# Optimization experiments

Measured on AMD Instinct MI355X. Metric: run time of the kernel, lower is better.

The kernel has to match this reference:

```python
import jax, jax.numpy as jnp
import numpy as np

B = 262144   # batch of candidate user-item pairs
D = 256      # concat embedding dim (embedding_dim*8)
H = 128      # hypernet hidden
HD = 32      # expert hidden dim
E = 4        # num experts


def setup_inputs() -> dict:
    key = jax.random.key(0)
    ks = jax.random.split(key, 16)
    def w(k, shape, fan_in):
        return jax.random.normal(k, shape, jnp.float32) * (1.0 / np.sqrt(fan_in))
    return {
        "x": jax.random.normal(ks[0], (B, D), jnp.float32),
        "context_embed": jax.random.normal(ks[1], (D,), jnp.float32),
        # hypernet (soft_module_route)
        "W1": w(ks[2], (D, H), D),   "b1": jnp.zeros((H,), jnp.float32),
        "W2": w(ks[3], (H, H), H),   "b2": jnp.zeros((H,), jnp.float32),
        "W12": w(ks[4], (H, E * E), H), "b12": jnp.zeros((E * E,), jnp.float32),
        "W22": w(ks[5], (H, E), H),     "b22": jnp.zeros((E,), jnp.float32),
        # soft_module experts: stacked per-expert Linear weights
        "Wf1": w(ks[6], (E, D, HD), D), "bf1": jnp.zeros((E, HD), jnp.float32),
        "Wf2": w(ks[7], (E, HD, HD), HD), "bf2": jnp.zeros((E, HD), jnp.float32),
        "Wfin": w(ks[8], (HD, 1), HD),  "bfin": jnp.zeros((1,), jnp.float32),
    }


def reference(x, context_embed, W1, b1, W2, b2, W12, b12, W22, b22,
              Wf1, bf1, Wf2, bf2, Wfin, bfin):
    # hypernet: routing weights from x * context
    embeds = x * context_embed[None, :]                       # [B,D]
    h = jax.nn.relu(embeds @ W1 + b1)                         # [B,H]
    c1 = jax.nn.softmax((h @ W12 + b12).reshape(-1, E, E), axis=1)   # [B,4,4]
    h2 = jax.nn.relu(h @ W2 + b2)                             # [B,H]
    c2 = jax.nn.softmax((h2 @ W22 + b22).reshape(-1, E, 1), axis=1)  # [B,4,1]
    # soft_module: 4 experts per layer, soft combined via c1/c2
    o1 = jax.nn.relu(jnp.einsum('bd,edh->bhe', x, Wf1) + bf1.T)      # [B,HD,E]
    in2 = jnp.einsum('bhe,bef->bhf', o1, c1)                         # [B,HD,E]
    o2 = jax.nn.relu(jnp.einsum('bhe,ehk->bke', in2, Wf2) + bf2.T)   # [B,HD,E]
    in3 = jnp.einsum('bke,bef->bkf', o2, c2)[..., 0]                 # [B,HD]
    return in3 @ Wfin + bfin                                         # [B,1]
```

## Files before the change

kernel.cpp:

```cpp
#include <hip/hip_runtime.h>
#include <hip/hip_bf16.h>

typedef _Float16 f16;
typedef _Float16 half8 __attribute__((ext_vector_type(8)));
typedef _Float16 half4 __attribute__((ext_vector_type(4)));
typedef float floatx4 __attribute__((ext_vector_type(4)));

#define BM 64

#define WA_OFF 0
#define WB_OFF 65536
#define WC_OFF 83968
#define WF2_OFF 86016
#define WSF_BYTE_OFF 180224
#define BA_OFF 0
#define BB_OFF 256
#define BCC_OFF 400
#define BF2_OFF 404
#define WFIN_OFF 532
#define BFIN_OFF 564

__global__ __launch_bounds__(256) void prep_kernel(
    const float* __restrict__ ctx, const float* __restrict__ W1,
    const float* __restrict__ b1, const float* __restrict__ W2,
    const float* __restrict__ b2, const float* __restrict__ W12,
    const float* __restrict__ b12, const float* __restrict__ W22,
    const float* __restrict__ b22, const float* __restrict__ Wf1,
    const float* __restrict__ bf1, const float* __restrict__ Wf2,
    const float* __restrict__ bf2, const float* __restrict__ Wfin,
    const float* __restrict__ bfin, f16* __restrict__ wsh,
    float* __restrict__ wsf)
{
  int tid = blockIdx.x * 256 + threadIdx.x;
  if (tid < 65536) {
    int j = tid & 7, l = (tid >> 3) & 63, kt = (tid >> 9) & 7, nt = tid >> 12;
    int k = kt * 32 + ((l >> 4) << 3) + j, n = nt * 16 + (l & 15);
    float v;
    if (n < 128) v = ctx[k] * W1[k * 128 + n];
    else { int c = n - 128; v = Wf1[((c >> 5) * 256 + k) * 32 + (c & 31)]; }
    wsh[tid] = (f16)v;
  } else if (tid < WB_OFF + 18432) {
    int o = tid - WB_OFF;
    int j = o & 7, l = (o >> 3) & 63, kt = (o >> 9) & 3, nt = o >> 11;
    int k = kt * 32 + ((l >> 4) << 3) + j, n = nt * 16 + (l & 15);
    float v = (n < 128) ? W2[k * 128 + n] : W12[k * 16 + (n - 128)];
    wsh[tid] = (f16)v;
  } else if (tid < WC_OFF + 2048) {
    int o = tid - WC_OFF;
    int j = o & 7, l = (o >> 3) & 63, kt = (o >> 9) & 3;
    int k = kt * 32 + ((l >> 4) << 3) + j, n = l & 15;
    float v = (n < 4) ? W22[k * 4 + n] : 0.f;
    wsh[tid] = (f16)v;
  } else if (tid < WF2_OFF + 4096) {
    int o = tid - WF2_OFF;
    int j = o & 7, l = (o >> 3) & 63, ent = o >> 9;
    int e = ent >> 1, nt = ent & 1;
    int k = ((l >> 4) << 3) + j, n = nt * 16 + (l & 15);
    wsh[tid] = (f16)Wf2[(e * 32 + k) * 32 + n];
  } else if (tid < 90112 + 565) {
    int o = tid - 90112;
    float v;
    if (o < 128) v = b1[o];
    else if (o < 256) v = bf1[o - 128];
    else if (o < 384) v = b2[o - 256];
    else if (o < 400) v = b12[o - 384];
    else if (o < 404) v = b22[o - 400];
    else if (o < 532) v = bf2[o - 404];
    else if (o < 564) v = Wfin[o - 532];
    else v = bfin[0];
    wsf[o] = v;
  }
}

#define MFMA16(A, Bv, C) __builtin_amdgcn_mfma_f32_16x16x32_f16(A, Bv, C, 0, 0, 0)

#define L1_OFF 32768
#define PART_OFF 32768
#define C2_OFF 34816

__global__ __launch_bounds__(256, 3) void fused_kernel(
    const float* __restrict__ x, const f16* __restrict__ wsh,
    const float* __restrict__ wsf, float* __restrict__ out)
{
  __shared__ __attribute__((aligned(16))) char lds[35840];
  const int t = threadIdx.x;
  const int lane = t & 63;
  const int w = t >> 6;
  const int l15 = lane & 15;
  const int l4 = lane >> 4;
  const size_t base = (size_t)blockIdx.x * BM;

#pragma unroll
  for (int it = 0; it < 8; ++it) {
    int c = it * 256 + t;
    int r = c >> 5;
    int k0 = (c & 31) << 3;
    const float4* xv = (const float4*)(x + (base + (size_t)r) * 256 + k0);
    float4 a = xv[0], b = xv[1];
    half8 hv;
    hv[0] = (f16)a.x; hv[1] = (f16)a.y; hv[2] = (f16)a.z; hv[3] = (f16)a.w;
    hv[4] = (f16)b.x; hv[5] = (f16)b.y; hv[6] = (f16)b.z; hv[7] = (f16)b.w;
    int addr = (r * 512 + k0 * 2) ^ ((r & 7) << 4);
    *(half8*)(lds + addr) = hv;
  }
  __syncthreads();

  {
    floatx4 acc[4][4];
#pragma unroll
    for (int q = 0; q < 4; ++q)
#pragma unroll
      for (int mt = 0; mt < 4; ++mt) acc[q][mt] = (floatx4){0.f, 0.f, 0.f, 0.f};
    for (int kt = 0; kt < 8; ++kt) {
      half8 Bx[4];
#pragma unroll
      for (int mt = 0; mt < 4; ++mt) {
        int r = mt * 16 + l15;
        int addr = (r * 512 + kt * 64 + (l4 << 4)) ^ ((r & 7) << 4);
        Bx[mt] = *(const half8*)(lds + addr);
      }
#pragma unroll
      for (int q = 0; q < 4; ++q) {
        half8 Wf = *(const half8*)(wsh + WA_OFF + (size_t)(((w * 4 + q) * 8 + kt) * 64 + lane) * 8);
#pragma unroll
        for (int mt = 0; mt < 4; ++mt) acc[q][mt] = MFMA16(Wf, Bx[mt], acc[q][mt]);
      }
    }
    __syncthreads();
#pragma unroll
    for (int q = 0; q < 4; ++q) {
      int c0 = (w * 4 + q) * 16 + l4 * 4;
      float4 bias = *(const float4*)(wsf + BA_OFF + c0);
#pragma unroll
      for (int mt = 0; mt < 4; ++mt) {
        int r = mt * 16 + l15;
        half4 hv;
#pragma unroll
        for (int i = 0; i < 4; ++i) hv[i] = (f16)fmaxf(acc[q][mt][i] + ((const float*)&bias)[i], 0.f);
        int addr = (r * 512 + c0 * 2) ^ ((r & 7) << 4);
        *(half4*)(lds + addr) = hv;
      }
    }
  }
  __syncthreads();

  {
    floatx4 acc2[2][4];
    floatx4 accL[4];
#pragma unroll
    for (int qi = 0; qi < 2; ++qi)
#pragma unroll
      for (int mt = 0; mt < 4; ++mt) acc2[qi][mt] = (floatx4){0.f, 0.f, 0.f, 0.f};
#pragma unroll
    for (int mt = 0; mt < 4; ++mt) accL[mt] = (floatx4){0.f, 0.f, 0.f, 0.f};

    for (int kt = 0; kt < 4; ++kt) {
      half8 Bh[4];
#pragma unroll
      for (int mt = 0; mt < 4; ++mt) {
        int r = mt * 16 + l15;
        int addr = (r * 512 + kt * 64 + (l4 << 4)) ^ ((r & 7) << 4);
        Bh[mt] = *(const half8*)(lds + addr);
      }
#pragma unroll
      for (int qi = 0; qi < 2; ++qi) {
        half8 Wf = *(const half8*)(wsh + WB_OFF + (size_t)(((w + qi * 4) * 4 + kt) * 64 + lane) * 8);
#pragma unroll
        for (int mt = 0; mt < 4; ++mt) acc2[qi][mt] = MFMA16(Wf, Bh[mt], acc2[qi][mt]);
      }
      if (w == 3) {
        half8 Wf = *(const half8*)(wsh + WB_OFF + (size_t)((32 + kt) * 64 + lane) * 8);
#pragma unroll
        for (int mt = 0; mt < 4; ++mt) accL[mt] = MFMA16(Wf, Bh[mt], accL[mt]);
      }
    }
    __syncthreads();
#pragma unroll
    for (int qi = 0; qi < 2; ++qi) {
      int c0 = (w + qi * 4) * 16 + l4 * 4;
      float4 bias = *(const float4*)(wsf + BB_OFF + c0);
#pragma unroll
      for (int mt = 0; mt < 4; ++mt) {
        int r = mt * 16 + l15;
        half4 hv;
#pragma unroll
        for (int i = 0; i < 4; ++i) hv[i] = (f16)fmaxf(acc2[qi][mt][i] + ((const float*)&bias)[i], 0.f);
        int addr = (r * 512 + c0 * 2) ^ ((r & 7) << 4);
        *(half4*)(lds + addr) = hv;
      }
    }
    if (w == 3) {
      int c0 = l4 * 4;
      float4 bias = *(const float4*)(wsf + BB_OFF + 128 + c0);
#pragma unroll
      for (int mt = 0; mt < 4; ++mt) {
        int r = mt * 16 + l15;
        half4 hv;
#pragma unroll
        for (int i = 0; i < 4; ++i) hv[i] = (f16)(accL[mt][i] + ((const float*)&bias)[i]);
        *(half4*)(lds + L1_OFF + r * 32 + c0 * 2) = hv;
      }
    }
  }
  __syncthreads();

  {
    floatx4 acc3 = (floatx4){0.f, 0.f, 0.f, 0.f};
    int r = w * 16 + l15;
#pragma unroll
    for (int kt = 0; kt < 4; ++kt) {
      int addr = (r * 512 + kt * 64 + (l4 << 4)) ^ ((r & 7) << 4);
      half8 Bh2 = *(const half8*)(lds + addr);
      half8 Wf = *(const half8*)(wsh + WC_OFF + (size_t)(kt * 64 + lane) * 8);
      acc3 = MFMA16(Wf, Bh2, acc3);
    }
    if (lane < 16) {
      float4 bias = *(const float4*)(wsf + BCC_OFF);
      float q0 = acc3[0] + bias.x, q1 = acc3[1] + bias.y;
      float q2 = acc3[2] + bias.z, q3 = acc3[3] + bias.w;
      float m2 = fmaxf(fmaxf(q0, q1), fmaxf(q2, q3));
      float f0 = __expf(q0 - m2), f1 = __expf(q1 - m2);
      float f2 = __expf(q2 - m2), f3 = __expf(q3 - m2);
      float inv2 = 1.f / (f0 + f1 + f2 + f3);
      float4 c2o;
      c2o.x = f0 * inv2; c2o.y = f1 * inv2; c2o.z = f2 * inv2; c2o.w = f3 * inv2;
      *(float4*)(lds + C2_OFF + r * 16) = c2o;
    }
  }

  {
    int r = t >> 2, f = t & 3;
    const f16* L1p = (const f16*)(lds + L1_OFF) + r * 16 + f;
    float a0 = (float)L1p[0], a1 = (float)L1p[4], a2 = (float)L1p[8], a3 = (float)L1p[12];
    float m = fmaxf(fmaxf(a0, a1), fmaxf(a2, a3));
    float e0 = __expf(a0 - m), e1 = __expf(a1 - m), e2 = __expf(a2 - m), e3 = __expf(a3 - m);
    float inv = 1.f / (e0 + e1 + e2 + e3);
    float c0v = e0 * inv, c1v = e1 * inv, c2v = e2 * inv, c3v = e3 * inv;
    int sw = (r & 7) << 4;
    half8 res[4];
#pragma unroll
    for (int h8 = 0; h8 < 4; ++h8) {
      half8 o0 = *(const half8*)(lds + ((r * 512 + 256 + 0   + h8 * 16) ^ sw));
      half8 o1v = *(const half8*)(lds + ((r * 512 + 256 + 64  + h8 * 16) ^ sw));
      half8 o2v = *(const half8*)(lds + ((r * 512 + 256 + 128 + h8 * 16) ^ sw));
      half8 o3v = *(const half8*)(lds + ((r * 512 + 256 + 192 + h8 * 16) ^ sw));
      half8 rr;
#pragma unroll
      for (int j = 0; j < 8; ++j) {
        float v = c0v * (float)o0[j] + c1v * (float)o1v[j] + c2v * (float)o2v[j] + c3v * (float)o3v[j];
        rr[j] = (f16)v;
      }
      res[h8] = rr;
    }
    __syncthreads();
#pragma unroll
    for (int h8 = 0; h8 < 4; ++h8)
      *(half8*)(lds + ((r * 512 + 256 + f * 64 + h8 * 16) ^ sw)) = res[h8];
  }
  __syncthreads();

  {
    floatx4 acc4[2][4];
#pragma unroll
    for (int ct = 0; ct < 2; ++ct)
#pragma unroll
      for (int mt = 0; mt < 4; ++mt) acc4[ct][mt] = (floatx4){0.f, 0.f, 0.f, 0.f};
    half8 Bi[4];
#pragma unroll
    for (int mt = 0; mt < 4; ++mt) {
      int r = mt * 16 + l15;
      int addr = (r * 512 + 256 + w * 64 + (l4 << 4)) ^ ((r & 7) << 4);
      Bi[mt] = *(const half8*)(lds + addr);
    }
#pragma unroll
    for (int ct = 0; ct < 2; ++ct) {
      half8 Wf = *(const half8*)(wsh + WF2_OFF + (size_t)((w * 2 + ct) * 64 + lane) * 8);
#pragma unroll
      for (int mt = 0; mt < 4; ++mt) acc4[ct][mt] = MFMA16(Wf, Bi[mt], acc4[ct][mt]);
    }
    float4 bias0 = *(const float4*)(wsf + BF2_OFF + w * 32 + l4 * 4);
    float4 bias1 = *(const float4*)(wsf + BF2_OFF + w * 32 + 16 + l4 * 4);
    float4 wf0 = *(const float4*)(wsf + WFIN_OFF + l4 * 4);
    float4 wf1 = *(const float4*)(wsf + WFIN_OFF + 16 + l4 * 4);
#pragma unroll
    for (int mt = 0; mt < 4; ++mt) {
      int r = mt * 16 + l15;
      float s = 0.f;
#pragma unroll
      for (int i = 0; i < 4; ++i) {
        s += fmaxf(acc4[0][mt][i] + ((const float*)&bias0)[i], 0.f) * ((const float*)&wf0)[i];
        s += fmaxf(acc4[1][mt][i] + ((const float*)&bias1)[i], 0.f) * ((const float*)&wf1)[i];
      }
      s += __shfl_xor(s, 16);
      s += __shfl_xor(s, 32);
      if (l4 == 0) {
        float c2e = *(const float*)(lds + C2_OFF + r * 16 + w * 4);
        *(float*)(lds + PART_OFF + (w * 64 + r) * 4) = s * c2e;
      }
    }
  }
  __syncthreads();

  if (t < 64) {
    float s = wsf[BFIN_OFF];
#pragma unroll
    for (int e = 0; e < 4; ++e) s += *(const float*)(lds + PART_OFF + e * 256 + t * 4);
    out[base + t] = s;
  }
}

extern "C" void kernel_launch(void* const* d_in, const int* in_sizes, int n_in,
                              void* d_out, int out_size, void* d_ws, size_t ws_size,
                              hipStream_t stream) {
  (void)in_sizes; (void)n_in; (void)ws_size;
  const float* x    = (const float*)d_in[0];
  const float* ctx  = (const float*)d_in[1];
  const float* W1   = (const float*)d_in[2];
  const float* b1   = (const float*)d_in[3];
  const float* W2   = (const float*)d_in[4];
  const float* b2   = (const float*)d_in[5];
  const float* W12  = (const float*)d_in[6];
  const float* b12  = (const float*)d_in[7];
  const float* W22  = (const float*)d_in[8];
  const float* b22  = (const float*)d_in[9];
  const float* Wf1  = (const float*)d_in[10];
  const float* bf1  = (const float*)d_in[11];
  const float* Wf2  = (const float*)d_in[12];
  const float* bf2  = (const float*)d_in[13];
  const float* Wfin = (const float*)d_in[14];
  const float* bfin = (const float*)d_in[15];

  f16* wsh = (f16*)d_ws;
  float* wsf = (float*)((char*)d_ws + WSF_BYTE_OFF);

  prep_kernel<<<355, 256, 0, stream>>>(ctx, W1, b1, W2, b2, W12, b12, W22, b22,
                                       Wf1, bf1, Wf2, bf2, Wfin, bfin, wsh, wsf);

  int nblocks = 262144 / BM;
  fused_kernel<<<nblocks, 256, 0, stream>>>(x, wsh, wsf, (float*)d_out);
}
```

Before: 112.9 us.

## Make each wave own 16 rows independently, eliminating block-wide barriers

```diff
diff --git a/kernel.cpp b/kernel.cpp
--- a/kernel.cpp
+++ b/kernel.cpp
@@ -74,238 +74,176 @@
 
 #define MFMA16(A, Bv, C) __builtin_amdgcn_mfma_f32_16x16x32_f16(A, Bv, C, 0, 0, 0)
 
-#define L1_OFF 32768
-#define PART_OFF 32768
-#define C2_OFF 34816
-
-__global__ __launch_bounds__(256, 3) void fused_kernel(
+#define WAVE_LDS 9216
+#define SCR_OFF 8192
+
+__global__ __launch_bounds__(256, 2) void fused_kernel(
     const float* __restrict__ x, const f16* __restrict__ wsh,
     const float* __restrict__ wsf, float* __restrict__ out)
 {
-  __shared__ __attribute__((aligned(16))) char lds[35840];
+  __shared__ __attribute__((aligned(16))) char lds[36864];
   const int t = threadIdx.x;
   const int lane = t & 63;
   const int w = t >> 6;
   const int l15 = lane & 15;
   const int l4 = lane >> 4;
-  const size_t base = (size_t)blockIdx.x * BM;
+  char* const wb = lds + w * WAVE_LDS;
+  const size_t base = (size_t)blockIdx.x * BM + (size_t)w * 16;
+  const int sw = (l15 & 7) << 4;
 
 #pragma unroll
   for (int it = 0; it < 8; ++it) {
-    int c = it * 256 + t;
-    int r = c >> 5;
-    int k0 = (c & 31) << 3;
-    const float4* xv = (const float4*)(x + (base + (size_t)r) * 256 + k0);
+    int rl = it * 2 + (lane >> 5);
+    int k0 = (lane & 31) << 3;
+    const float4* xv = (const float4*)(x + (base + (size_t)rl) * 256 + k0);
     float4 a = xv[0], b = xv[1];
     half8 hv;
     hv[0] = (f16)a.x; hv[1] = (f16)a.y; hv[2] = (f16)a.z; hv[3] = (f16)a.w;
     hv[4] = (f16)b.x; hv[5] = (f16)b.y; hv[6] = (f16)b.z; hv[7] = (f16)b.w;
-    int addr = (r * 512 + k0 * 2) ^ ((r & 7) << 4);
-    *(half8*)(lds + addr) = hv;
-  }
-  __syncthreads();
-
-  {
-    floatx4 acc[4][4];
-#pragma unroll
-    for (int q = 0; q < 4; ++q)
-#pragma unroll
-      for (int mt = 0; mt < 4; ++mt) acc[q][mt] = (floatx4){0.f, 0.f, 0.f, 0.f};
+    *(half8*)(wb + ((rl * 512 + k0 * 2) ^ ((rl & 7) << 4))) = hv;
+  }
+
+  {
+    floatx4 acc[16];
+#pragma unroll
+    for (int nt = 0; nt < 16; ++nt) acc[nt] = (floatx4){0.f, 0.f, 0.f, 0.f};
     for (int kt = 0; kt < 8; ++kt) {
-      half8 Bx[4];
-#pragma unroll
-      for (int mt = 0; mt < 4; ++mt) {
-        int r = mt * 16 + l15;
-        int addr = (r * 512 + kt * 64 + (l4 << 4)) ^ ((r & 7) << 4);
-        Bx[mt] = *(const half8*)(lds + addr);
+      half8 Bx = *(const half8*)(wb + ((l15 * 512 + kt * 64 + (l4 << 4)) ^ sw));
+#pragma unroll
+      for (int nt = 0; nt < 16; ++nt) {
+        half8 Wf = *(const half8*)(wsh + WA_OFF + (size_t)((nt * 8 + kt) * 64 + lane) * 8);
+        acc[nt] = MFMA16(Wf, Bx, acc[nt]);
       }
-#pragma unroll
-      for (int q = 0; q < 4; ++q) {
-        half8 Wf = *(const half8*)(wsh + WA_OFF + (size_t)(((w * 4 + q) * 8 + kt) * 64 + lane) * 8);
-#pragma unroll
-        for (int mt = 0; mt < 4; ++mt) acc[q][mt] = MFMA16(Wf, Bx[mt], acc[q][mt]);
+    }
+#pragma unroll
+    for (int nt = 0; nt < 16; ++nt) {
+      int c0 = nt * 16 + l4 * 4;
+      float4 bias = *(const float4*)(wsf + BA_OFF + c0);
+      half4 hv;
+#pragma unroll
+      for (int i = 0; i < 4; ++i) hv[i] = (f16)fmaxf(acc[nt][i] + ((const float*)&bias)[i], 0.f);
+      *(half4*)(wb + ((l15 * 512 + c0 * 2) ^ sw)) = hv;
+    }
+  }
+
+  float4 c1v;
+  {
+    floatx4 acc2[9];
+#pragma unroll
+    for (int nt = 0; nt < 9; ++nt) acc2[nt] = (floatx4){0.f, 0.f, 0.f, 0.f};
+    for (int kt = 0; kt < 4; ++kt) {
+      half8 Bh = *(const half8*)(wb + ((l15 * 512 + kt * 64 + (l4 << 4)) ^ sw));
+#pragma unroll
+      for (int nt = 0; nt < 9; ++nt) {
+        half8 Wf = *(const half8*)(wsh + WB_OFF + (size_t)((nt * 4 + kt) * 64 + lane) * 8);
+        acc2[nt] = MFMA16(Wf, Bh, acc2[nt]);
       }
     }
-    __syncthreads();
-#pragma unroll
-    for (int q = 0; q < 4; ++q) {
-      int c0 = (w * 4 + q) * 16 + l4 * 4;
-      float4 bias = *(const float4*)(wsf + BA_OFF + c0);
-#pragma unroll
-      for (int mt = 0; mt < 4; ++mt) {
-        int r = mt * 16 + l15;
-        half4 hv;
-#pragma unroll
-        for (int i = 0; i < 4; ++i) hv[i] = (f16)fmaxf(acc[q][mt][i] + ((const float*)&bias)[i], 0.f);
-        int addr = (r * 512 + c0 * 2) ^ ((r & 7) << 4);
-        *(half4*)(lds + addr) = hv;
-      }
-    }
-  }
-  __syncthreads();
-
-  {
-    floatx4 acc2[2][4];
-    floatx4 accL[4];
-#pragma unroll
-    for (int qi = 0; qi < 2; ++qi)
-#pragma unroll
-      for (int mt = 0; mt < 4; ++mt) acc2[qi][mt] = (floatx4){0.f, 0.f, 0.f, 0.f};
-#pragma unroll
-    for (int mt = 0; mt < 4; ++mt) accL[mt] = (floatx4){0.f, 0.f, 0.f, 0.f};
-
+#pragma unroll
+    for (int nt = 0; nt < 8; ++nt) {
+      int c0 = nt * 16 + l4 * 4;
+      float4 bias = *(const float4*)(wsf + BB_OFF + c0);
+      half4 hv;
+#pragma unroll
+      for (int i = 0; i < 4; ++i) hv[i] = (f16)fmaxf(acc2[nt][i] + ((const float*)&bias)[i], 0.f);
+      *(half4*)(wb + ((l15 * 512 + c0 * 2) ^ sw)) = hv;
+    }
+    float4 biasL = *(const float4*)(wsf + BB_OFF + 128 + l4 * 4);
+    float lg[4], mx[4];
+#pragma unroll
+    for (int i = 0; i < 4; ++i) lg[i] = acc2[8][i] + ((const float*)&biasL)[i];
+#pragma unroll
+    for (int i = 0; i < 4; ++i) {
+      float m = lg[i];
+      m = fmaxf(m, __shfl_xor(m, 16));
+      m = fmaxf(m, __shfl_xor(m, 32));
+      mx[i] = m;
+    }
+    float ex[4], sm[4];
+#pragma unroll
+    for (int i = 0; i < 4; ++i) {
+      ex[i] = __expf(lg[i] - mx[i]);
+      float s = ex[i];
+      s += __shfl_xor(s, 16);
+      s += __shfl_xor(s, 32);
+      sm[i] = s;
+    }
+#pragma unroll
+    for (int i = 0; i < 4; ++i) ((float*)&c1v)[i] = ex[i] / sm[i];
+  }
+
+  f16 c1h[4];
+  {
+    *(float4*)(wb + SCR_OFF + l15 * 64 + l4 * 16) = c1v;
+#pragma unroll
+    for (int j = 0; j < 4; ++j)
+      c1h[j] = (f16)(*(const float*)(wb + SCR_OFF + l15 * 64 + j * 16 + l4 * 4));
+  }
+
+  float4 c2v;
+  {
+    floatx4 acc3 = (floatx4){0.f, 0.f, 0.f, 0.f};
+#pragma unroll
     for (int kt = 0; kt < 4; ++kt) {
-      half8 Bh[4];
-#pragma unroll
-      for (int mt = 0; mt < 4; ++mt) {
-        int r = mt * 16 + l15;
-        int addr = (r * 512 + kt * 64 + (l4 << 4)) ^ ((r & 7) << 4);
-        Bh[mt] = *(const half8*)(lds + addr);
-      }
-#pragma unroll
-      for (int qi = 0; qi < 2; ++qi) {
-        half8 Wf = *(const half8*)(wsh + WB_OFF + (size_t)(((w + qi * 4) * 4 + kt) * 64 + lane) * 8);
-#pragma unroll
-        for (int mt = 0; mt < 4; ++mt) acc2[qi][mt] = MFMA16(Wf, Bh[mt], acc2[qi][mt]);
-      }
-      if (w == 3) {
-        half8 Wf = *(const half8*)(wsh + WB_OFF + (size_t)((32 + kt) * 64 + lane) * 8);
-#pragma unroll
-        for (int mt = 0; mt < 4; ++mt) accL[mt] = MFMA16(Wf, Bh[mt], accL[mt]);
-      }
-    }
-    __syncthreads();
-#pragma unroll
-    for (int qi = 0; qi < 2; ++qi) {
-      int c0 = (w + qi * 4) * 16 + l4 * 4;
-      float4 bias = *(const float4*)(wsf + BB_OFF + c0);
-#pragma unroll
-      for (int mt = 0; mt < 4; ++mt) {
-        int r = mt * 16 + l15;
-        half4 hv;
-#pragma unroll
-        for (int i = 0; i < 4; ++i) hv[i] = (f16)fmaxf(acc2[qi][mt][i] + ((const float*)&bias)[i], 0.f);
-        int addr = (r * 512 + c0 * 2) ^ ((r & 7) << 4);
-        *(half4*)(lds + addr) = hv;
-      }
-    }
-    if (w == 3) {
-      int c0 = l4 * 4;
-      float4 bias = *(const float4*)(wsf + BB_OFF + 128 + c0);
-#pragma unroll
-      for (int mt = 0; mt < 4; ++mt) {
-        int r = mt * 16 + l15;
-        half4 hv;
-#pragma unroll
-        for (int i = 0; i < 4; ++i) hv[i] = (f16)(accL[mt][i] + ((const float*)&bias)[i]);
-        *(half4*)(lds + L1_OFF + r * 32 + c0 * 2) = hv;
-      }
-    }
-  }
-  __syncthreads();
-
-  {
-    floatx4 acc3 = (floatx4){0.f, 0.f, 0.f, 0.f};
-    int r = w * 16 + l15;
-#pragma unroll
-    for (int kt = 0; kt < 4; ++kt) {
-      int addr = (r * 512 + kt * 64 + (l4 << 4)) ^ ((r & 7) << 4);
-      half8 Bh2 = *(const half8*)(lds + addr);
+      half8 Bh2 = *(const half8*)(wb + ((l15 * 512 + kt * 64 + (l4 << 4)) ^ sw));
       half8 Wf = *(const half8*)(wsh + WC_OFF + (size_t)(kt * 64 + lane) * 8);
       acc3 = MFMA16(Wf, Bh2, acc3);
     }
-    if (lane < 16) {
-      float4 bias = *(const float4*)(wsf + BCC_OFF);
-      float q0 = acc3[0] + bias.x, q1 = acc3[1] + bias.y;
-      float q2 = acc3[2] + bias.z, q3 = acc3[3] + bias.w;
-      float m2 = fmaxf(fmaxf(q0, q1), fmaxf(q2, q3));
-      float f0 = __expf(q0 - m2), f1 = __expf(q1 - m2);
-      float f2 = __expf(q2 - m2), f3 = __expf(q3 - m2);
-      float inv2 = 1.f / (f0 + f1 + f2 + f3);
-      float4 c2o;
-      c2o.x = f0 * inv2; c2o.y = f1 * inv2; c2o.z = f2 * inv2; c2o.w = f3 * inv2;
-      *(float4*)(lds + C2_OFF + r * 16) = c2o;
-    }
-  }
-
-  {
-    int r = t >> 2, f = t & 3;
-    const f16* L1p = (const f16*)(lds + L1_OFF) + r * 16 + f;
-    float a0 = (float)L1p[0], a1 = (float)L1p[4], a2 = (float)L1p[8], a3 = (float)L1p[12];
-    float m = fmaxf(fmaxf(a0, a1), fmaxf(a2, a3));
-    float e0 = __expf(a0 - m), e1 = __expf(a1 - m), e2 = __expf(a2 - m), e3 = __expf(a3 - m);
-    float inv = 1.f / (e0 + e1 + e2 + e3);
-    float c0v = e0 * inv, c1v = e1 * inv, c2v = e2 * inv, c3v = e3 * inv;
-    int sw = (r & 7) << 4;
+    float4 bias = *(const float4*)(wsf + BCC_OFF);
+    float q0 = acc3[0] + bias.x, q1 = acc3[1] + bias.y;
+    float q2 = acc3[2] + bias.z, q3 = acc3[3] + bias.w;
+    float m2 = fmaxf(fmaxf(q0, q1), fmaxf(q2, q3));
+    float f0 = __expf(q0 - m2), f1 = __expf(q1 - m2);
+    float f2 = __expf(q2 - m2), f3 = __expf(q3 - m2);
+    float inv2 = 1.f / (f0 + f1 + f2 + f3);
+    c2v.x = f0 * inv2; c2v.y = f1 * inv2; c2v.z = f2 * inv2; c2v.w = f3 * inv2;
+  }
+
+  {
     half8 res[4];
 #pragma unroll
     for (int h8 = 0; h8 < 4; ++h8) {
-      half8 o0 = *(const half8*)(lds + ((r * 512 + 256 + 0   + h8 * 16) ^ sw));
-      half8 o1v = *(const half8*)(lds + ((r * 512 + 256 + 64  + h8 * 16) ^ sw));
-      half8 o2v = *(const half8*)(lds + ((r * 512 + 256 + 128 + h8 * 16) ^ sw));
-      half8 o3v = *(const half8*)(lds + ((r * 512 + 256 + 192 + h8 * 16) ^ sw));
-      half8 rr;
-#pragma unroll
-      for (int j = 0; j < 8; ++j) {
-        float v = c0v * (float)o0[j] + c1v * (float)o1v[j] + c2v * (float)o2v[j] + c3v * (float)o3v[j];
-        rr[j] = (f16)v;
-      }
-      res[h8] = rr;
-    }
-    __syncthreads();
+      half8 o0 = *(const half8*)(wb + ((l15 * 512 + 256 + 0   + h8 * 16) ^ sw));
+      half8 o1v = *(const half8*)(wb + ((l15 * 512 + 256 + 64  + h8 * 16) ^ sw));
+      half8 o2v = *(const half8*)(wb + ((l15 * 512 + 256 + 128 + h8 * 16) ^ sw));
+      half8 o3v = *(const half8*)(wb + ((l15 * 512 + 256 + 192 + h8 * 16) ^ sw));
+      half8 r = o0 * c1h[0];
+      r = r + o1v * c1h[1];
+      r = r + o2v * c1h[2];
+      r = r + o3v * c1h[3];
+      res[h8] = r;
+    }
 #pragma unroll
     for (int h8 = 0; h8 < 4; ++h8)
-      *(half8*)(lds + ((r * 512 + 256 + f * 64 + h8 * 16) ^ sw)) = res[h8];
-  }
-  __syncthreads();
-
-  {
-    floatx4 acc4[2][4];
-#pragma unroll
-    for (int ct = 0; ct < 2; ++ct)
-#pragma unroll
-      for (int mt = 0; mt < 4; ++mt) acc4[ct][mt] = (floatx4){0.f, 0.f, 0.f, 0.f};
-    half8 Bi[4];
-#pragma unroll
-    for (int mt = 0; mt < 4; ++mt) {
-      int r = mt * 16 + l15;
-      int addr = (r * 512 + 256 + w * 64 + (l4 << 4)) ^ ((r & 7) << 4);
-      Bi[mt] = *(const half8*)(lds + addr);
-    }
-#pragma unroll
-    for (int ct = 0; ct < 2; ++ct) {
-      half8 Wf = *(const half8*)(wsh + WF2_OFF + (size_t)((w * 2 + ct) * 64 + lane) * 8);
-#pragma unroll
-      for (int mt = 0; mt < 4; ++mt) acc4[ct][mt] = MFMA16(Wf, Bi[mt], acc4[ct][mt]);
-    }
-    float4 bias0 = *(const float4*)(wsf + BF2_OFF + w * 32 + l4 * 4);
-    float4 bias1 = *(const float4*)(wsf + BF2_OFF + w * 32 + 16 + l4 * 4);
+      *(half8*)(wb + ((l15 * 512 + 256 + l4 * 64 + h8 * 16) ^ sw)) = res[h8];
+  }
+
+  {
     float4 wf0 = *(const float4*)(wsf + WFIN_OFF + l4 * 4);
     float4 wf1 = *(const float4*)(wsf + WFIN_OFF + 16 + l4 * 4);
-#pragma unroll
-    for (int mt = 0; mt < 4; ++mt) {
-      int r = mt * 16 + l15;
+    float total = 0.f;
+#pragma unroll
+    for (int e = 0; e < 4; ++e) {
+      half8 Bi = *(const half8*)(wb + ((l15 * 512 + 256 + e * 64 + (l4 << 4)) ^ sw));
+      floatx4 a0 = (floatx4){0.f, 0.f, 0.f, 0.f}, a1 = a0;
+      half8 Wf0v = *(const half8*)(wsh + WF2_OFF + (size_t)((e * 2 + 0) * 64 + lane) * 8);
+      half8 Wf1v = *(const half8*)(wsh + WF2_OFF + (size_t)((e * 2 + 1) * 64 + lane) * 8);
+      a0 = MFMA16(Wf0v, Bi, a0);
+      a1 = MFMA16(Wf1v, Bi, a1);
+      float4 b0 = *(const float4*)(wsf + BF2_OFF + e * 32 + l4 * 4);
+      float4 b1 = *(const float4*)(wsf + BF2_OFF + e * 32 + 16 + l4 * 4);
       float s = 0.f;
 #pragma unroll
       for (int i = 0; i < 4; ++i) {
-        s += fmaxf(acc4[0][mt][i] + ((const float*)&bias0)[i], 0.f) * ((const float*)&wf0)[i];
-        s += fmaxf(acc4[1][mt][i] + ((const float*)&bias1)[i], 0.f) * ((const float*)&wf1)[i];
+        s += fmaxf(a0[i] + ((const float*)&b0)[i], 0.f) * ((const float*)&wf0)[i];
+        s += fmaxf(a1[i] + ((const float*)&b1)[i], 0.f) * ((const float*)&wf1)[i];
       }
       s += __shfl_xor(s, 16);
       s += __shfl_xor(s, 32);
-      if (l4 == 0) {
-        float c2e = *(const float*)(lds + C2_OFF + r * 16 + w * 4);
-        *(float*)(lds + PART_OFF + (w * 64 + r) * 4) = s * c2e;
-      }
-    }
-  }
-  __syncthreads();
-
-  if (t < 64) {
-    float s = wsf[BFIN_OFF];
-#pragma unroll
-    for (int e = 0; e < 4; ++e) s += *(const float*)(lds + PART_OFF + e * 256 + t * 4);
-    out[base + t] = s;
+      float c2e = __shfl(((const float*)&c2v)[e], l15);
+      total += s * c2e;
+    }
+    if (l4 == 0) out[base + l15] = total + wsf[BFIN_OFF];
   }
 }
 
```

Measured after the change: 283.9 us. 151% more time.

## Split fused MoE kernel work across 8 waves per block with separate H2 buffer

Applied to the files above, without the earlier changes.

```diff
diff --git a/kernel.cpp b/kernel.cpp
--- a/kernel.cpp
+++ b/kernel.cpp
@@ -74,25 +74,27 @@
 
 #define MFMA16(A, Bv, C) __builtin_amdgcn_mfma_f32_16x16x32_f16(A, Bv, C, 0, 0, 0)
 
-#define L1_OFF 32768
-#define PART_OFF 32768
-#define C2_OFF 34816
-
-__global__ __launch_bounds__(256, 3) void fused_kernel(
+#define H2_OFF 32768
+#define L1_OFF 49152
+#define PART_OFF 49152
+#define C2_OFF 51200
+
+__global__ __launch_bounds__(512, 6) void fused_kernel(
     const float* __restrict__ x, const f16* __restrict__ wsh,
     const float* __restrict__ wsf, float* __restrict__ out)
 {
-  __shared__ __attribute__((aligned(16))) char lds[35840];
+  __shared__ __attribute__((aligned(16))) char lds[52224];
   const int t = threadIdx.x;
   const int lane = t & 63;
   const int w = t >> 6;
   const int l15 = lane & 15;
   const int l4 = lane >> 4;
+  const int sw = (l15 & 7) << 4;
   const size_t base = (size_t)blockIdx.x * BM;
 
 #pragma unroll
-  for (int it = 0; it < 8; ++it) {
-    int c = it * 256 + t;
+  for (int it = 0; it < 4; ++it) {
+    int c = it * 512 + t;
     int r = c >> 5;
     int k0 = (c & 31) << 3;
     const float4* xv = (const float4*)(x + (base + (size_t)r) * 256 + k0);
@@ -100,15 +102,14 @@
     half8 hv;
     hv[0] = (f16)a.x; hv[1] = (f16)a.y; hv[2] = (f16)a.z; hv[3] = (f16)a.w;
     hv[4] = (f16)b.x; hv[5] = (f16)b.y; hv[6] = (f16)b.z; hv[7] = (f16)b.w;
-    int addr = (r * 512 + k0 * 2) ^ ((r & 7) << 4);
-    *(half8*)(lds + addr) = hv;
+    *(half8*)(lds + ((r * 512 + k0 * 2) ^ ((r & 7) << 4))) = hv;
   }
   __syncthreads();
 
   {
-    floatx4 acc[4][4];
-#pragma unroll
-    for (int q = 0; q < 4; ++q)
+    floatx4 acc[2][4];
+#pragma unroll
+    for (int q = 0; q < 2; ++q)
 #pragma unroll
       for (int mt = 0; mt < 4; ++mt) acc[q][mt] = (floatx4){0.f, 0.f, 0.f, 0.f};
     for (int kt = 0; kt < 8; ++kt) {
@@ -116,20 +117,19 @@
 #pragma unroll
       for (int mt = 0; mt < 4; ++mt) {
         int r = mt * 16 + l15;
-        int addr = (r * 512 + kt * 64 + (l4 << 4)) ^ ((r & 7) << 4);
-        Bx[mt] = *(const half8*)(lds + addr);
-      }
-#pragma unroll
-      for (int q = 0; q < 4; ++q) {
-        half8 Wf = *(const half8*)(wsh + WA_OFF + (size_t)(((w * 4 + q) * 8 + kt) * 64 + lane) * 8);
+        Bx[mt] = *(const half8*)(lds + ((r * 512 + kt * 64 + (l4 << 4)) ^ sw));
+      }
+#pragma unroll
+      for (int q = 0; q < 2; ++q) {
+        half8 Wf = *(const half8*)(wsh + WA_OFF + (size_t)(((w * 2 + q) * 8 + kt) * 64 + lane) * 8);
 #pragma unroll
         for (int mt = 0; mt < 4; ++mt) acc[q][mt] = MFMA16(Wf, Bx[mt], acc[q][mt]);
       }
     }
     __syncthreads();
 #pragma unroll
-    for (int q = 0; q < 4; ++q) {
-      int c0 = (w * 4 + q) * 16 + l4 * 4;
+    for (int q = 0; q < 2; ++q) {
+      int c0 = (w * 2 + q) * 16 + l4 * 4;
       float4 bias = *(const float4*)(wsf + BA_OFF + c0);
 #pragma unroll
       for (int mt = 0; mt < 4; ++mt) {
@@ -137,80 +137,68 @@
         half4 hv;
 #pragma unroll
         for (int i = 0; i < 4; ++i) hv[i] = (f16)fmaxf(acc[q][mt][i] + ((const float*)&bias)[i], 0.f);
-        int addr = (r * 512 + c0 * 2) ^ ((r & 7) << 4);
-        *(half4*)(lds + addr) = hv;
+        *(half4*)(lds + ((r * 512 + c0 * 2) ^ sw)) = hv;
       }
     }
   }
   __syncthreads();
 
   {
-    floatx4 acc2[2][4];
+    floatx4 acc2[4];
     floatx4 accL[4];
 #pragma unroll
-    for (int qi = 0; qi < 2; ++qi)
-#pragma unroll
-      for (int mt = 0; mt < 4; ++mt) acc2[qi][mt] = (floatx4){0.f, 0.f, 0.f, 0.f};
-#pragma unroll
-    for (int mt = 0; mt < 4; ++mt) accL[mt] = (floatx4){0.f, 0.f, 0.f, 0.f};
-
+    for (int mt = 0; mt < 4; ++mt) {
+      acc2[mt] = (floatx4){0.f, 0.f, 0.f, 0.f};
+      accL[mt] = (floatx4){0.f, 0.f, 0.f, 0.f};
+    }
     for (int kt = 0; kt < 4; ++kt) {
       half8 Bh[4];
 #pragma unroll
       for (int mt = 0; mt < 4; ++mt) {
         int r = mt * 16 + l15;
-        int addr = (r * 512 + kt * 64 + (l4 << 4)) ^ ((r & 7) << 4);
-        Bh[mt] = *(const half8*)(lds + addr);
-      }
-#pragma unroll
-      for (int qi = 0; qi < 2; ++qi) {
-        half8 Wf = *(const half8*)(wsh + WB_OFF + (size_t)(((w + qi * 4) * 4 + kt) * 64 + lane) * 8);
-#pragma unroll
-        for (int mt = 0; mt < 4; ++mt) acc2[qi][mt] = MFMA16(Wf, Bh[mt], acc2[qi][mt]);
-      }
-      if (w == 3) {
-        half8 Wf = *(const half8*)(wsh + WB_OFF + (size_t)((32 + kt) * 64 + lane) * 8);
-#pragma unroll
-        for (int mt = 0; mt < 4; ++mt) accL[mt] = MFMA16(Wf, Bh[mt], accL[mt]);
-      }
-    }
-    __syncthreads();
-#pragma unroll
-    for (int qi = 0; qi < 2; ++qi) {
-      int c0 = (w + qi * 4) * 16 + l4 * 4;
+        Bh[mt] = *(const half8*)(lds + ((r * 512 + kt * 64 + (l4 << 4)) ^ sw));
+      }
+      half8 Wf = *(const half8*)(wsh + WB_OFF + (size_t)((w * 4 + kt) * 64 + lane) * 8);
+#pragma unroll
+      for (int mt = 0; mt < 4; ++mt) acc2[mt] = MFMA16(Wf, Bh[mt], acc2[mt]);
+      if (w == 7) {
+        half8 WfL = *(const half8*)(wsh + WB_OFF + (size_t)((32 + kt) * 64 + lane) * 8);
+#pragma unroll
+        for (int mt = 0; mt < 4; ++mt) accL[mt] = MFMA16(WfL, Bh[mt], accL[mt]);
+      }
+    }
+    {
+      int c0 = w * 16 + l4 * 4;
       float4 bias = *(const float4*)(wsf + BB_OFF + c0);
 #pragma unroll
       for (int mt = 0; mt < 4; ++mt) {
         int r = mt * 16 + l15;
         half4 hv;
 #pragma unroll
-        for (int i = 0; i < 4; ++i) hv[i] = (f16)fmaxf(acc2[qi][mt][i] + ((const float*)&bias)[i], 0.f);
-        int addr = (r * 512 + c0 * 2) ^ ((r & 7) << 4);
-        *(half4*)(lds + addr) = hv;
-      }
-    }
-    if (w == 3) {
-      int c0 = l4 * 4;
-      float4 bias = *(const float4*)(wsf + BB_OFF + 128 + c0);
+        for (int i = 0; i < 4; ++i) hv[i] = (f16)fmaxf(acc2[mt][i] + ((const float*)&bias)[i], 0.f);
+        *(half4*)(lds + H2_OFF + ((r * 256 + c0 * 2) ^ ((r & 7) << 4))) = hv;
+      }
+    }
+    if (w == 7) {
+      float4 biasL = *(const float4*)(wsf + BB_OFF + 128 + l4 * 4);
 #pragma unroll
       for (int mt = 0; mt < 4; ++mt) {
         int r = mt * 16 + l15;
         half4 hv;
 #pragma unroll
-        for (int i = 0; i < 4; ++i) hv[i] = (f16)(accL[mt][i] + ((const float*)&bias)[i]);
-        *(half4*)(lds + L1_OFF + r * 32 + c0 * 2) = hv;
-      }
-    }
-  }
-  __syncthreads();
-
-  {
+        for (int i = 0; i < 4; ++i) hv[i] = (f16)(accL[mt][i] + ((const float*)&biasL)[i]);
+        *(half4*)(lds + L1_OFF + r * 32 + l4 * 8) = hv;
+      }
+    }
+  }
+  __syncthreads();
+
+  if (w < 4) {
     floatx4 acc3 = (floatx4){0.f, 0.f, 0.f, 0.f};
-    int r = w * 16 + l15;
+    int r3 = w * 16 + l15;
 #pragma unroll
     for (int kt = 0; kt < 4; ++kt) {
-      int addr = (r * 512 + kt * 64 + (l4 << 4)) ^ ((r & 7) << 4);
-      half8 Bh2 = *(const half8*)(lds + addr);
+      half8 Bh2 = *(const half8*)(lds + H2_OFF + ((r3 * 256 + kt * 64 + (l4 << 4)) ^ ((r3 & 7) << 4)));
       half8 Wf = *(const half8*)(wsh + WC_OFF + (size_t)(kt * 64 + lane) * 8);
       acc3 = MFMA16(Wf, Bh2, acc3);
     }
@@ -224,88 +212,67 @@
       float inv2 = 1.f / (f0 + f1 + f2 + f3);
       float4 c2o;
       c2o.x = f0 * inv2; c2o.y = f1 * inv2; c2o.z = f2 * inv2; c2o.w = f3 * inv2;
-      *(float4*)(lds + C2_OFF + r * 16) = c2o;
-    }
-  }
-
+      *(float4*)(lds + C2_OFF + r3 * 16) = c2o;
+    }
+  }
   {
-    int r = t >> 2, f = t & 3;
+    int r = t >> 3, f = (t >> 1) & 3, hh = t & 1;
     const f16* L1p = (const f16*)(lds + L1_OFF) + r * 16 + f;
     float a0 = (float)L1p[0], a1 = (float)L1p[4], a2 = (float)L1p[8], a3 = (float)L1p[12];
     float m = fmaxf(fmaxf(a0, a1), fmaxf(a2, a3));
     float e0 = __expf(a0 - m), e1 = __expf(a1 - m), e2 = __expf(a2 - m), e3 = __expf(a3 - m);
     float inv = 1.f / (e0 + e1 + e2 + e3);
-    float c0v = e0 * inv, c1v = e1 * inv, c2v = e2 * inv, c3v = e3 * inv;
-    int sw = (r & 7) << 4;
-    half8 res[4];
-#pragma unroll
-    for (int h8 = 0; h8 < 4; ++h8) {
-      half8 o0 = *(const half8*)(lds + ((r * 512 + 256 + 0   + h8 * 16) ^ sw));
-      half8 o1v = *(const half8*)(lds + ((r * 512 + 256 + 64  + h8 * 16) ^ sw));
-      half8 o2v = *(const half8*)(lds + ((r * 512 + 256 + 128 + h8 * 16) ^ sw));
-      half8 o3v = *(const half8*)(lds + ((r * 512 + 256 + 192 + h8 * 16) ^ sw));
-      half8 rr;
-#pragma unroll
-      for (int j = 0; j < 8; ++j) {
-        float v = c0v * (float)o0[j] + c1v * (float)o1v[j] + c2v * (float)o2v[j] + c3v * (float)o3v[j];
-        rr[j] = (f16)v;
-      }
-      res[h8] = rr;
-    }
-    __syncthreads();
-#pragma unroll
-    for (int h8 = 0; h8 < 4; ++h8)
-      *(half8*)(lds + ((r * 512 + 256 + f * 64 + h8 * 16) ^ sw)) = res[h8];
+    f16 c0h = (f16)(e0 * inv), c1h = (f16)(e1 * inv);
+    f16 c2h = (f16)(e2 * inv), c3h = (f16)(e3 * inv);
+    int swr = (r & 7) << 4;
+#pragma unroll
+    for (int hi = 0; hi < 2; ++hi) {
+      int h8 = hh * 2 + hi;
+      half8 o0 = *(const half8*)(lds + ((r * 512 + 256 + 0   + h8 * 16) ^ swr));
+      half8 o1v = *(const half8*)(lds + ((r * 512 + 256 + 64  + h8 * 16) ^ swr));
+      half8 o2v = *(const half8*)(lds + ((r * 512 + 256 + 128 + h8 * 16) ^ swr));
+      half8 o3v = *(const half8*)(lds + ((r * 512 + 256 + 192 + h8 * 16) ^ swr));
+      half8 res = o0 * c0h + o1v * c1h + o2v * c2h + o3v * c3h;
+      *(half8*)(lds + ((r * 512 + f * 64 + h8 * 16) ^ swr)) = res;
+    }
   }
   __syncthreads();
 
   {
-    floatx4 acc4[2][4];
-#pragma unroll
-    for (int ct = 0; ct < 2; ++ct)
-#pragma unroll
-      for (int mt = 0; mt < 4; ++mt) acc4[ct][mt] = (floatx4){0.f, 0.f, 0.f, 0.f};
-    half8 Bi[4];
+    int e = w & 3, ct = w >> 2;
+    half8 Wfv = *(const half8*)(wsh + WF2_OFF + (size_t)((e * 2 + ct) * 64 + lane) * 8);
+    float4 bv = *(const float4*)(wsf + BF2_OFF + e * 32 + ct * 16 + l4 * 4);
+    float4 wfv = *(const float4*)(wsf + WFIN_OFF + ct * 16 + l4 * 4);
+    floatx4 a4[4];
+#pragma unroll
+    for (int mt = 0; mt < 4; ++mt) a4[mt] = (floatx4){0.f, 0.f, 0.f, 0.f};
 #pragma unroll
     for (int mt = 0; mt < 4; ++mt) {
       int r = mt * 16 + l15;
-      int addr = (r * 512 + 256 + w * 64 + (l4 << 4)) ^ ((r & 7) << 4);
-      Bi[mt] = *(const half8*)(lds + addr);
-    }
-#pragma unroll
-    for (int ct = 0; ct < 2; ++ct) {
-      half8 Wf = *(const half8*)(wsh + WF2_OFF + (size_t)((w * 2 + ct) * 64 + lane) * 8);
-#pragma unroll
-      for (int mt = 0; mt < 4; ++mt) acc4[ct][mt] = MFMA16(Wf, Bi[mt], acc4[ct][mt]);
-    }
-    float4 bias0 = *(const float4*)(wsf + BF2_OFF + w * 32 + l4 * 4);
-    float4 bias1 = *(const float4*)(wsf + BF2_OFF + w * 32 + 16 + l4 * 4);
-    float4 wf0 = *(const float4*)(wsf + WFIN_OFF + l4 * 4);
-    float4 wf1 = *(const float4*)(wsf + WFIN_OFF + 16 + l4 * 4);
+      half8 Bi = *(const half8*)(lds + ((r * 512 + e * 64 + (l4 << 4)) ^ ((r & 7) << 4)));
+      a4[mt] = MFMA16(Wfv, Bi, a4[mt]);
+    }
 #pragma unroll
     for (int mt = 0; mt < 4; ++mt) {
       int r = mt * 16 + l15;
       float s = 0.f;
 #pragma unroll
-      for (int i = 0; i < 4; ++i) {
-        s += fmaxf(acc4[0][mt][i] + ((const float*)&bias0)[i], 0.f) * ((const float*)&wf0)[i];
-        s += fmaxf(acc4[1][mt][i] + ((const float*)&bias1)[i], 0.f) * ((const float*)&wf1)[i];
-      }
+      for (int i = 0; i < 4; ++i)
+        s += fmaxf(a4[mt][i] + ((const float*)&bv)[i], 0.f) * ((const float*)&wfv)[i];
       s += __shfl_xor(s, 16);
       s += __shfl_xor(s, 32);
       if (l4 == 0) {
-        float c2e = *(const float*)(lds + C2_OFF + r * 16 + w * 4);
-        *(float*)(lds + PART_OFF + (w * 64 + r) * 4) = s * c2e;
+        float c2e = *(const float*)(lds + C2_OFF + r * 16 + e * 4);
+        *(float*)(lds + PART_OFF + r * 32 + w * 4) = s * c2e;
       }
     }
   }
   __syncthreads();
 
   if (t < 64) {
-    float s = wsf[BFIN_OFF];
-#pragma unroll
-    for (int e = 0; e < 4; ++e) s += *(const float*)(lds + PART_OFF + e * 256 + t * 4);
-    out[base + t] = s;
+    float4 p0 = *(const float4*)(lds + PART_OFF + t * 32);
+    float4 p1 = *(const float4*)(lds + PART_OFF + t * 32 + 16);
+    out[base + t] = wsf[BFIN_OFF] + p0.x + p0.y + p0.z + p0.w + p1.x + p1.y + p1.z + p1.w;
   }
 }
 
@@ -337,5 +304,5 @@
                                        Wf1, bf1, Wf2, bf2, Wfin, bfin, wsh, wsf);
 
   int nblocks = 262144 / BM;
-  fused_kernel<<<nblocks, 256, 0, stream>>>(x, wsh, wsf, (float*)d_out);
+  fused_kernel<<<nblocks, 512, 0, stream>>>(x, wsh, wsf, (float*)d_out);
 }
```

After: 118.2 us. 4.6% more time.
